# Optimization experiments

Measured on AMD Instinct MI355X. Metric: run time of the kernel, lower is better.

## Reference

```python
import jax, jax.numpy as jnp
import numpy as np

H = 4  # fixed number of heads in the layer


def setup_inputs() -> dict:
    key = jax.random.key(0)
    ks = jax.random.split(key, 6)
    B, S, D = 4, 2048, 512
    U = 2 * D  # per-head projection width (units = d_model * 2)
    x = jax.random.normal(ks[0], (B, S, D), dtype=jnp.float32)
    gamma = jnp.ones((D,), dtype=jnp.float32)
    beta = jnp.zeros((D,), dtype=jnp.float32)
    s = 0.02
    Wq = jax.random.normal(ks[1], (H, D, U), dtype=jnp.float32) * s
    Wk = jax.random.normal(ks[2], (H, D, U), dtype=jnp.float32) * s
    Wv = jax.random.normal(ks[3], (H, D, U), dtype=jnp.float32) * s
    Wout = jax.random.normal(ks[4], (H * U, D), dtype=jnp.float32) * s
    return {"x": x, "gamma": gamma, "beta": beta, "Wq": Wq, "Wk": Wk, "Wv": Wv, "Wout": Wout}


def _forward(x, gamma, beta, Wq, Wk, Wv, Wout):
    B, S, D = x.shape
    eps = 1e-6
    # LayerNormalization over last axis (Keras default, eps=1e-6)
    mu = jnp.mean(x, axis=-1, keepdims=True)
    var = jnp.mean(jnp.square(x - mu), axis=-1, keepdims=True)
    xn = (x - mu) * jax.lax.rsqrt(var + eps) * gamma + beta
    # Per-head Q/K/V projections, batched over head axis. Dropout is identity at inference.
    q = jnp.einsum('bsd,hdu->bhsu', xn, Wq)
    k = jnp.einsum('bsd,hdu->bhsu', xn, Wk)
    v = jnp.einsum('bsd,hdu->bhsu', xn, Wv)
    # Keras Attention(use_scale=False, causal=True): unscaled dot-product scores
    scores = jnp.einsum('bhsu,bhtu->bhst', q, k)  # [B,H,S,S]
    causal = jnp.tril(jnp.ones((S, S), dtype=bool))
    scores = jnp.where(causal, scores, jnp.finfo(scores.dtype).min)
    probs = jax.nn.softmax(scores, axis=-1)
    head = jnp.einsum('bhst,bhtu->bhsu', probs, v)  # [B,H,S,U]
    # concat heads in head order -> [B,S,H*U], then output Dense back to D
    HU = head.shape[1] * head.shape[3]
    cat = head.transpose(0, 2, 1, 3).reshape(B, S, HU)
    return cat @ Wout


def reference(x, gamma, beta, Wq, Wk, Wv, Wout):
    return _forward(x, gamma, beta, Wq, Wk, Wv, Wout)
```

## Files before the change

### kernel.cpp

```cpp
#include <hip/hip_runtime.h>

typedef _Float16 half8 __attribute__((ext_vector_type(8)));
typedef float floatx4 __attribute__((ext_vector_type(4)));

__device__ __forceinline__ void gl16(const _Float16* g, _Float16* l) {
    __builtin_amdgcn_global_load_lds((const __attribute__((address_space(1))) void*)g,
                                     (__attribute__((address_space(3))) void*)l, 16, 0, 0);
}

__device__ __forceinline__ half8 dsr16(const _Float16* p) {
    half8 r;
    const __attribute__((address_space(3))) _Float16* lp =
        (const __attribute__((address_space(3))) _Float16*)p;
    asm volatile("ds_read_b128 %0, %1" : "=v"(r) : "v"(lp));
    return r;
}

#define Scst 2048
#define Dcst 512
#define Ucst 1024
#define Hcst 4
#define SDo 1048576LL
#define UDo 524288LL
#define SUo 2097152LL
#define SSo 4194304LL
#define USo 2097152LL
#define SHUo 8388608LL

__global__ __launch_bounds__(64) void ln_k(const float* __restrict__ x,
                                           const float* __restrict__ gamma,
                                           const float* __restrict__ beta,
                                           _Float16* __restrict__ xn) {
    const int D = 512;
    long long base = (long long)blockIdx.x * D;
    int lane = threadIdx.x;
    floatx4 x0 = *(const floatx4*)(x + base + lane * 8);
    floatx4 x1 = *(const floatx4*)(x + base + lane * 8 + 4);
    float f[8];
#pragma unroll
    for (int i = 0; i < 4; i++) { f[i] = x0[i]; f[4 + i] = x1[i]; }
    float s = 0.f, ss = 0.f;
#pragma unroll
    for (int i = 0; i < 8; i++) { s += f[i]; ss += f[i] * f[i]; }
#pragma unroll
    for (int off = 32; off; off >>= 1) { s += __shfl_xor(s, off); ss += __shfl_xor(ss, off); }
    float mean = s * (1.f / 512.f);
    float var = ss * (1.f / 512.f) - mean * mean;
    float rstd = rsqrtf(var + 1e-6f);
    floatx4 g0 = *(const floatx4*)(gamma + lane * 8);
    floatx4 g1 = *(const floatx4*)(gamma + lane * 8 + 4);
    floatx4 b0 = *(const floatx4*)(beta + lane * 8);
    floatx4 b1 = *(const floatx4*)(beta + lane * 8 + 4);
    half8 o;
#pragma unroll
    for (int i = 0; i < 4; i++) {
        o[i]     = (_Float16)((f[i]     - mean) * rstd * g0[i] + b0[i]);
        o[4 + i] = (_Float16)((f[4 + i] - mean) * rstd * g1[i] + b1[i]);
    }
    *(half8*)(xn + base + lane * 8) = o;
}

__global__ __launch_bounds__(256) void tr_k(const float* __restrict__ in,
                                            _Float16* __restrict__ out, int R, int C) {
    __shared__ _Float16 tile[32][33];
    int tx = threadIdx.x, ty = threadIdx.y;
    long long zo = (long long)blockIdx.z * R * C;
    int r0 = blockIdx.y * 32, c0 = blockIdx.x * 32;
    for (int yy = ty; yy < 32; yy += 8)
        tile[yy][tx] = (_Float16)in[zo + (long long)(r0 + yy) * C + c0 + tx];
    __syncthreads();
    for (int yy = ty; yy < 32; yy += 8)
        out[zo + (long long)(c0 + yy) * R + r0 + tx] = tile[tx][yy];
}

#define BM 128
#define BN 128
#define BK 32
__global__ __launch_bounds__(256) void gemm_bt(
    const _Float16* __restrict__ A, const _Float16* __restrict__ Bt, void* __restrict__ Cv,
    int K, int ldc, int cflags, int mode) {
    int z = blockIdx.z;
    long long offA = 0, offB = 0, offC = 0;
    switch (mode) {
        case 1:
            offA = (long long)((z >> 2) & 1) * SDo;
            offB = (long long)(((z >> 3) * 4) + (z & 3)) * UDo;
            offC = (long long)(((z >> 3) * 8) + ((z & 3) * 2) + ((z >> 2) & 1)) * SUo;
            break;
        case 2:
            offA = (long long)z * SUo; offB = (long long)z * SUo; offC = (long long)z * SSo;
            break;
        case 3:
            offA = (long long)(z >> 1) * UDo; offB = (long long)(z & 1) * SDo;
            offC = (long long)z * USo;
            break;
        case 4:
            offA = (long long)z * SSo; offB = (long long)z * USo;
            offC = (long long)(z & 1) * SHUo + (long long)(z >> 1) * Ucst;
            break;
        case 6:
            offB = (long long)(z & 7) * UDo; offC = (long long)z * SUo;
            break;
        case 7:
            offA = (long long)(z & 3) * UDo; offC = (long long)z * USo;
            break;
        default: break;
    }
    const _Float16* Ab = A + offA;
    const _Float16* Bb = Bt + offB;

    int gx = gridDim.x, gy = gridDim.y;
    int nb = gx * gy;
    int lin = blockIdx.y * gx + blockIdx.x;
    int mIdx, nIdx;
    if (((nb & 7) == 0) && ((gx & 3) == 0)) {
        int chunk = nb >> 3;
        int vid = (lin >> 3) + chunk * (lin & 7);
        int panelH = gy * 4;
        int panel = vid / panelH;
        int rem = vid - panel * panelH;
        mIdx = rem >> 2;
        nIdx = (panel << 2) + (rem & 3);
    } else { mIdx = blockIdx.y; nIdx = blockIdx.x; }
    int m0 = mIdx * BM, n0 = nIdx * BN;

    if ((cflags & 4) && n0 > m0 + (BM - 1)) return;
    int kend = (cflags & 8) ? min(K, m0 + BM) : K;

    __shared__ _Float16 As[2][BM * BK];
    __shared__ _Float16 Bs[2][BN * BK];

    int t = threadIdx.x;
    int srow = t >> 2;
    int scol = (t & 3) * 8;
    int lane = t & 63, w = t >> 6;
    int wm = (w >> 1) * 64, wn = (w & 1) * 64;
    int lm = lane & 15, lk = (lane >> 4) * 8;

    floatx4 acc[4][4];
#pragma unroll
    for (int i = 0; i < 4; i++)
#pragma unroll
        for (int j = 0; j < 4; j++) acc[i][j] = floatx4{0.f, 0.f, 0.f, 0.f};

    const _Float16* ga0 = Ab + (long long)(m0 + srow) * K + scol;
    const _Float16* ga1 = Ab + (long long)(m0 + 64 + srow) * K + scol;
    const _Float16* gb0 = Bb + (long long)(n0 + srow) * K + scol;
    const _Float16* gb1 = Bb + (long long)(n0 + 64 + srow) * K + scol;

    int nIter = kend / BK;
    gl16(ga0, &As[0][t * 8]);
    gl16(ga1, &As[0][2048 + t * 8]);
    gl16(gb0, &Bs[0][t * 8]);
    gl16(gb1, &Bs[0][2048 + t * 8]);

    for (int it = 0; it < nIter; it++) {
        __syncthreads();
        int cur = it & 1;
        half8 af[4], bfr[4];
#pragma unroll
        for (int i = 0; i < 4; i++) af[i] = *(const half8*)&As[cur][(wm + i * 16 + lm) * BK + lk];
#pragma unroll
        for (int j = 0; j < 4; j++) bfr[j] = *(const half8*)&Bs[cur][(wn + j * 16 + lm) * BK + lk];
        if (it + 1 < nIter) {
            int nk = (it + 1) * BK;
            int nxt = cur ^ 1;
            gl16(ga0 + nk, &As[nxt][t * 8]);
            gl16(ga1 + nk, &As[nxt][2048 + t * 8]);
            gl16(gb0 + nk, &Bs[nxt][t * 8]);
            gl16(gb1 + nk, &Bs[nxt][2048 + t * 8]);
        }
#pragma unroll
        for (int i = 0; i < 4; i++)
#pragma unroll
            for (int j = 0; j < 4; j++)
                acc[i][j] = __builtin_amdgcn_mfma_f32_16x16x32_f16(af[i], bfr[j], acc[i][j], 0, 0, 0);
    }

    int cr = (lane >> 4) * 4;
    int cc = lm;
    bool outf32 = (cflags & 1) != 0;
#pragma unroll
    for (int i = 0; i < 4; i++) {
#pragma unroll
        for (int j = 0; j < 4; j++) {
            int rr = m0 + wm + i * 16 + cr;
            int nn = n0 + wn + j * 16 + cc;
#pragma unroll
            for (int r2 = 0; r2 < 4; r2++) {
                long long idx = (long long)(rr + r2) * ldc + nn + offC;
                float val = acc[i][j][r2];
                if (outf32) ((float*)Cv)[idx] = val;
                else ((_Float16*)Cv)[idx] = (_Float16)val;
            }
        }
    }
}

__global__ __launch_bounds__(512, 2) void gemm_bt256(
    const _Float16* __restrict__ A, const _Float16* __restrict__ Bt, void* __restrict__ Cv,
    int K, int ldc, int cflags, int mode) {
    int z = blockIdx.z;
    long long offA = 0, offB = 0, offC = 0;
    switch (mode) {
        case 1:
            offA = (long long)((z >> 2) & 1) * SDo;
            offB = (long long)(((z >> 3) * 4) + (z & 3)) * UDo;
            offC = (long long)(((z >> 3) * 8) + ((z & 3) * 2) + ((z >> 2) & 1)) * SUo;
            break;
        case 2:
            offA = (long long)z * SUo; offB = (long long)z * SUo; offC = (long long)z * SSo;
            break;
        case 3:
            offA = (long long)(z >> 1) * UDo; offB = (long long)(z & 1) * SDo;
            offC = (long long)z * USo;
            break;
        case 4:
            offA = (long long)z * SSo; offB = (long long)z * USo;
            offC = (long long)(z & 1) * SHUo + (long long)(z >> 1) * Ucst;
            break;
        default: break;
    }
    const _Float16* Ab = A + offA;
    const _Float16* Bb = Bt + offB;

    int gx = gridDim.x;
    int nwg = gx * gridDim.y;
    int lin = blockIdx.y * gx + blockIdx.x;
    int q8 = nwg >> 3, r8 = nwg & 7;
    int xcd = lin & 7, sub8 = lin >> 3;
    int wg = (xcd < r8 ? xcd * (q8 + 1) : r8 * (q8 + 1) + (xcd - r8) * q8) + sub8;
    int m0 = (wg / gx) * 256, n0 = (wg % gx) * 256;

    if ((cflags & 4) && n0 > m0 + 255) return;
    int kend = (cflags & 8) ? min(K, m0 + 256) : K;
    int NT = kend >> 6;

    __shared__ _Float16 As2[2][2][8192];
    __shared__ _Float16 Bs2[2][2][8192];

    int t = threadIdx.x;
    int lane = t & 63, w = t >> 6;
    int wm = (w >> 2) * 128, wn = (w & 3) * 64;
    int lm = lane & 15, ls = lane >> 4;
    int sw8 = ((ls ^ ((lm >> 1) & 3)) << 3);

    long long stoff = (long long)(t >> 2) * K + (((t & 3) ^ ((t >> 3) & 3)) << 3);
    const _Float16* gA = Ab + (long long)m0 * K + stoff;
    const _Float16* gB = Bb + (long long)n0 * K + stoff;
    long long rowK = 128LL * K;
    int ldd = t * 8;

    floatx4 acc[8][4];
#pragma unroll
    for (int i = 0; i < 8; i++)
#pragma unroll
        for (int j = 0; j < 4; j++) acc[i][j] = floatx4{0.f, 0.f, 0.f, 0.f};

#define STGA(v, ks) { const _Float16* s_ = gA + (((v) << 6) + ((ks) << 5)); \
        gl16(s_, &As2[(v) & 1][ks][ldd]); gl16(s_ + rowK, &As2[(v) & 1][ks][4096 + ldd]); }
#define STGB(v, ks) { const _Float16* s_ = gB + (((v) << 6) + ((ks) << 5)); \
        gl16(s_, &Bs2[(v) & 1][ks][ldd]); gl16(s_ + rowK, &Bs2[(v) & 1][ks][4096 + ldd]); }
#define RDA(mm, ks) dsr16(&As2[cur][ks][(wm + (mm) * 16 + lm) * 32 + sw8])
#define RDB(nn, ks) dsr16(&Bs2[cur][ks][(wn + (nn) * 16 + lm) * 32 + sw8])
#define MFMAH(m0_, m1_) \
    _Pragma("unroll") for (int mm = (m0_); mm < (m1_); mm++) \
    _Pragma("unroll") for (int nn = 0; nn < 4; nn++) \
        acc[mm][nn] = __builtin_amdgcn_mfma_f32_16x16x32_f16( \
            af[mm], bf[nn], acc[mm][nn], 0, 0, 0);

    STGA(0, 0) STGB(0, 0) STGA(0, 1) STGB(0, 1) STGA(1, 0) STGB(1, 0)
    asm volatile("s_waitcnt vmcnt(8)" ::: "memory");
    __builtin_amdgcn_s_barrier();

    for (int tt = 0; tt < NT; tt++) {
        int cur = tt & 1;
        half8 af[8], bf[4];
        bool more = (tt + 1 < NT);
        bf[0] = RDB(0, 0); bf[1] = RDB(1, 0); bf[2] = RDB(2, 0); bf[3] = RDB(3, 0);
        af[0] = RDA(0, 0); af[1] = RDA(1, 0); af[2] = RDA(2, 0); af[3] = RDA(3, 0);
        af[4] = RDA(4, 0); af[5] = RDA(5, 0); af[6] = RDA(6, 0); af[7] = RDA(7, 0);
        if (more) asm volatile("s_waitcnt vmcnt(4)" ::: "memory");
        else      asm volatile("s_waitcnt vmcnt(0)" ::: "memory");
        __builtin_amdgcn_s_barrier();
        asm volatile("s_waitcnt lgkmcnt(4)" ::: "memory");
        __builtin_amdgcn_sched_barrier(0);
        __builtin_amdgcn_s_setprio(1);
        MFMAH(0, 4)
        asm volatile("s_waitcnt lgkmcnt(0)" ::: "memory");
        __builtin_amdgcn_sched_barrier(0);
        MFMAH(4, 8)
        __builtin_amdgcn_s_setprio(0);
        if (more) { STGA(tt + 1, 1) STGB(tt + 1, 1) }
        bf[0] = RDB(0, 1); bf[1] = RDB(1, 1); bf[2] = RDB(2, 1); bf[3] = RDB(3, 1);
        af[0] = RDA(0, 1); af[1] = RDA(1, 1); af[2] = RDA(2, 1); af[3] = RDA(3, 1);
        af[4] = RDA(4, 1); af[5] = RDA(5, 1); af[6] = RDA(6, 1); af[7] = RDA(7, 1);
        if (more) asm volatile("s_waitcnt vmcnt(4)" ::: "memory");
        else      asm volatile("s_waitcnt vmcnt(0)" ::: "memory");
        __builtin_amdgcn_s_barrier();
        asm volatile("s_waitcnt lgkmcnt(4)" ::: "memory");
        __builtin_amdgcn_sched_barrier(0);
        __builtin_amdgcn_s_setprio(1);
        MFMAH(0, 4)
        asm volatile("s_waitcnt lgkmcnt(0)" ::: "memory");
        __builtin_amdgcn_sched_barrier(0);
        MFMAH(4, 8)
        __builtin_amdgcn_s_setprio(0);
        if (tt + 2 < NT) { STGA(tt + 2, 0) STGB(tt + 2, 0) }
    }

    int cr = ls * 4, cc = lm;
    bool outf32 = (cflags & 1) != 0;
#pragma unroll
    for (int i = 0; i < 8; i++) {
#pragma unroll
        for (int j = 0; j < 4; j++) {
            int rr = m0 + wm + i * 16 + cr;
            int nn = n0 + wn + j * 16 + cc;
#pragma unroll
            for (int r2 = 0; r2 < 4; r2++) {
                long long idx = (long long)(rr + r2) * ldc + nn + offC;
                float val = acc[i][j][r2];
                if (outf32) ((float*)Cv)[idx] = val;
                else ((_Float16*)Cv)[idx] = (_Float16)val;
            }
        }
    }
#undef STGA
#undef STGB
#undef RDA
#undef RDB
#undef MFMAH
}

__global__ __launch_bounds__(256) void softmax_h(_Float16* __restrict__ sc, int S) {
    int wid = threadIdx.x >> 6, lane = threadIdx.x & 63;
    int idx = blockIdx.x * 4 + wid;
    int r = idx & (S - 1);
    _Float16* srow = sc + (long long)idx * S;
    int nc = r >> 9;
    float v[32];
    float mx = -3.0e38f;
    for (int c = 0; c <= nc; c++) {
        half8 hv = *(half8*)(srow + lane * 8 + c * 512);
#pragma unroll
        for (int i = 0; i < 8; i++) {
            int n = lane * 8 + c * 512 + i;
            float s = (n <= r) ? (float)hv[i] : -3.0e38f;
            v[c * 8 + i] = s; mx = fmaxf(mx, s);
        }
    }
#pragma unroll
    for (int off = 32; off; off >>= 1) mx = fmaxf(mx, __shfl_xor(mx, off));
    float sum = 0.f;
    for (int c = 0; c <= nc; c++)
#pragma unroll
        for (int i = 0; i < 8; i++) {
            int n = lane * 8 + c * 512 + i;
            float e = (n <= r) ? __expf(v[c * 8 + i] - mx) : 0.f;
            v[c * 8 + i] = e; sum += e;
        }
#pragma unroll
    for (int off = 32; off; off >>= 1) sum += __shfl_xor(sum, off);
    float inv = 1.f / sum;
    for (int c = 0; c <= nc; c++) {
        half8 o;
#pragma unroll
        for (int i = 0; i < 8; i++) o[i] = (_Float16)(v[c * 8 + i] * inv);
        *(half8*)(srow + lane * 8 + c * 512) = o;
    }
}

extern "C" void kernel_launch(void* const* d_in, const int* in_sizes, int n_in,
                              void* d_out, int out_size, void* d_ws, size_t ws_size,
                              hipStream_t stream) {
    const int B = 4, S = 2048, D = 512, H = 4, U = 1024;
    const float* x     = (const float*)d_in[0];
    const float* gamma = (const float*)d_in[1];
    const float* beta  = (const float*)d_in[2];
    const float* Wq    = (const float*)d_in[3];
    const float* Wk    = (const float*)d_in[4];
    const float* Wv    = (const float*)d_in[5];
    const float* Wout  = (const float*)d_in[6];
    float* out = (float*)d_out;

    char* ws = (char*)d_ws;
    const size_t MiB = 1ull << 20;
    const long long SD = SDo, UD = UDo, SU = SUo, US = USo;

    _Float16* xn  = (_Float16*)(ws + 0);
    _Float16* WqT = (_Float16*)(ws + 8  * MiB);
    _Float16* WkT = (_Float16*)(ws + 12 * MiB);
    _Float16* WvT = (_Float16*)(ws + 16 * MiB);
    _Float16* WoT = (_Float16*)(ws + 20 * MiB);

    tr_k<<<dim3(U / 32, D / 32, H), dim3(32, 8), 0, stream>>>(Wq, WqT, D, U);
    tr_k<<<dim3(U / 32, D / 32, H), dim3(32, 8), 0, stream>>>(Wk, WkT, D, U);
    tr_k<<<dim3(U / 32, D / 32, H), dim3(32, 8), 0, stream>>>(Wv, WvT, D, U);
    tr_k<<<dim3(D / 32, (H * U) / 32, 1), dim3(32, 8), 0, stream>>>(Wout, WoT, H * U, D);
    ln_k<<<B * S, 64, 0, stream>>>(x, gamma, beta, xn);

    if (ws_size >= 168 * MiB) {
        _Float16* qk  = (_Float16*)(ws + 24 * MiB);
        _Float16* kk  = qk + 8 * SU;
        _Float16* sc  = (_Float16*)(ws + 88 * MiB);
        _Float16* vt  = qk;
        _Float16* cat = kk;

        for (int p = 0; p < 2; p++) {
            const _Float16* xnp = xn + (long long)p * 2 * SD;
            float* outp = out + (long long)p * 2 * SD;
            gemm_bt256<<<dim3(U / 256, S / 256, 16), 512, 0, stream>>>(xnp, WqT, qk, D, U, 0, 1);
            gemm_bt256<<<dim3(S / 256, S / 256, 8), 512, 0, stream>>>(qk, kk, sc, U, S, 4, 2);
            softmax_h<<<8 * S / 4, 256, 0, stream>>>(sc, S);
            gemm_bt256<<<dim3(S / 256, U / 256, 8), 512, 0, stream>>>(WvT, xnp, vt, D, S, 0, 3);
            gemm_bt256<<<dim3(U / 256, S / 256, 8), 512, 0, stream>>>(sc, vt, cat, S, H * U, 8, 4);
            gemm_bt<<<dim3(D / 128, 2 * S / 128, 1), 256, 0, stream>>>(cat, WoT, outp,
                H * U, D, 1, 0);
        }
    } else {
        _Float16* qb   = (_Float16*)(ws + 24 * MiB);
        _Float16* vTb  = (_Float16*)(ws + 56 * MiB);
        _Float16* catb = (_Float16*)(ws + 72 * MiB);
        _Float16* sc   = (_Float16*)(ws + 88 * MiB);

        for (int b = 0; b < B; b++) {
            const _Float16* xnb = xn + (long long)b * SD;
            gemm_bt<<<dim3(U / 128, S / 128, 2 * H), 256, 0, stream>>>(xnb, WqT, qb, D, U, 0, 6);
            gemm_bt<<<dim3(S / 128, U / 128, H), 256, 0, stream>>>(WvT, xnb, vTb, D, S, 0, 7);
            for (int h = 0; h < H; h++) {
                gemm_bt<<<dim3(S / 128, S / 128, 1), 256, 0, stream>>>(qb + (long long)h * SU,
                    qb + (long long)(H + h) * SU, sc, U, S, 4, 0);
                softmax_h<<<S / 4, 256, 0, stream>>>(sc, S);
                gemm_bt<<<dim3(U / 128, S / 128, 1), 256, 0, stream>>>(sc,
                    vTb + (long long)h * US, (void*)(catb + (long long)h * U), S, H * U, 8, 0);
            }
            gemm_bt<<<dim3(D / 128, S / 128, 1), 256, 0, stream>>>(catb, WoT,
                (void*)(out + (long long)b * SD), H * U, D, 1, 0);
        }
    }
}
```

Measured before the change: 696.5 us.

## Stage GEMM epilogue through LDS for coalesced fp16 stores and reorder prefetch

```diff
diff --git a/kernel.cpp b/kernel.cpp
--- a/kernel.cpp
+++ b/kernel.cpp
@@ -6,14 +6,6 @@
 __device__ __forceinline__ void gl16(const _Float16* g, _Float16* l) {
     __builtin_amdgcn_global_load_lds((const __attribute__((address_space(1))) void*)g,
                                      (__attribute__((address_space(3))) void*)l, 16, 0, 0);
-}
-
-__device__ __forceinline__ half8 dsr16(const _Float16* p) {
-    half8 r;
-    const __attribute__((address_space(3))) _Float16* lp =
-        (const __attribute__((address_space(3))) _Float16*)p;
-    asm volatile("ds_read_b128 %0, %1" : "=v"(r) : "v"(lp));
-    return r;
 }
 
 #define Scst 2048
@@ -236,8 +228,9 @@
     int kend = (cflags & 8) ? min(K, m0 + 256) : K;
     int NT = kend >> 6;
 
-    __shared__ _Float16 As2[2][2][8192];
-    __shared__ _Float16 Bs2[2][2][8192];
+    __shared__ _Float16 SH[65536];
+#define ASX(b, k, i) SH[((b) << 14) + ((k) << 13) + (i)]
+#define BSX(b, k, i) SH[32768 + ((b) << 14) + ((k) << 13) + (i)]
 
     int t = threadIdx.x;
     int lane = t & 63, w = t >> 6;
@@ -258,13 +251,13 @@
         for (int j = 0; j < 4; j++) acc[i][j] = floatx4{0.f, 0.f, 0.f, 0.f};
 
 #define STGA(v, ks) { const _Float16* s_ = gA + (((v) << 6) + ((ks) << 5)); \
-        gl16(s_, &As2[(v) & 1][ks][ldd]); gl16(s_ + rowK, &As2[(v) & 1][ks][4096 + ldd]); }
+        gl16(s_, &ASX((v) & 1, ks, ldd)); gl16(s_ + rowK, &ASX((v) & 1, ks, 4096 + ldd)); }
 #define STGB(v, ks) { const _Float16* s_ = gB + (((v) << 6) + ((ks) << 5)); \
-        gl16(s_, &Bs2[(v) & 1][ks][ldd]); gl16(s_ + rowK, &Bs2[(v) & 1][ks][4096 + ldd]); }
-#define RDA(mm, ks) dsr16(&As2[cur][ks][(wm + (mm) * 16 + lm) * 32 + sw8])
-#define RDB(nn, ks) dsr16(&Bs2[cur][ks][(wn + (nn) * 16 + lm) * 32 + sw8])
-#define MFMAH(m0_, m1_) \
-    _Pragma("unroll") for (int mm = (m0_); mm < (m1_); mm++) \
+        gl16(s_, &BSX((v) & 1, ks, ldd)); gl16(s_ + rowK, &BSX((v) & 1, ks, 4096 + ldd)); }
+#define RDA(mm, ks) (*(const half8*)&ASX(cur, ks, (wm + (mm) * 16 + lm) * 32 + sw8))
+#define RDB(nn, ks) (*(const half8*)&BSX(cur, ks, (wn + (nn) * 16 + lm) * 32 + sw8))
+#define MFMA32() \
+    _Pragma("unroll") for (int mm = 0; mm < 8; mm++) \
     _Pragma("unroll") for (int nn = 0; nn < 4; nn++) \
         acc[mm][nn] = __builtin_amdgcn_mfma_f32_16x16x32_f16( \
             af[mm], bf[nn], acc[mm][nn], 0, 0, 0);
@@ -275,62 +268,66 @@
 
     for (int tt = 0; tt < NT; tt++) {
         int cur = tt & 1;
-        half8 af[8], bf[4];
         bool more = (tt + 1 < NT);
-        bf[0] = RDB(0, 0); bf[1] = RDB(1, 0); bf[2] = RDB(2, 0); bf[3] = RDB(3, 0);
-        af[0] = RDA(0, 0); af[1] = RDA(1, 0); af[2] = RDA(2, 0); af[3] = RDA(3, 0);
-        af[4] = RDA(4, 0); af[5] = RDA(5, 0); af[6] = RDA(6, 0); af[7] = RDA(7, 0);
-        if (more) asm volatile("s_waitcnt vmcnt(4)" ::: "memory");
-        else      asm volatile("s_waitcnt vmcnt(0)" ::: "memory");
-        __builtin_amdgcn_s_barrier();
-        asm volatile("s_waitcnt lgkmcnt(4)" ::: "memory");
-        __builtin_amdgcn_sched_barrier(0);
-        __builtin_amdgcn_s_setprio(1);
-        MFMAH(0, 4)
-        asm volatile("s_waitcnt lgkmcnt(0)" ::: "memory");
-        __builtin_amdgcn_sched_barrier(0);
-        MFMAH(4, 8)
-        __builtin_amdgcn_s_setprio(0);
-        if (more) { STGA(tt + 1, 1) STGB(tt + 1, 1) }
-        bf[0] = RDB(0, 1); bf[1] = RDB(1, 1); bf[2] = RDB(2, 1); bf[3] = RDB(3, 1);
-        af[0] = RDA(0, 1); af[1] = RDA(1, 1); af[2] = RDA(2, 1); af[3] = RDA(3, 1);
-        af[4] = RDA(4, 1); af[5] = RDA(5, 1); af[6] = RDA(6, 1); af[7] = RDA(7, 1);
-        if (more) asm volatile("s_waitcnt vmcnt(4)" ::: "memory");
-        else      asm volatile("s_waitcnt vmcnt(0)" ::: "memory");
-        __builtin_amdgcn_s_barrier();
-        asm volatile("s_waitcnt lgkmcnt(4)" ::: "memory");
-        __builtin_amdgcn_sched_barrier(0);
-        __builtin_amdgcn_s_setprio(1);
-        MFMAH(0, 4)
-        asm volatile("s_waitcnt lgkmcnt(0)" ::: "memory");
-        __builtin_amdgcn_sched_barrier(0);
-        MFMAH(4, 8)
-        __builtin_amdgcn_s_setprio(0);
-        if (tt + 2 < NT) { STGA(tt + 2, 0) STGB(tt + 2, 0) }
-    }
-
-    int cr = ls * 4, cc = lm;
-    bool outf32 = (cflags & 1) != 0;
+        {
+            half8 af[8], bf[4];
+            bf[0] = RDB(0, 0); bf[1] = RDB(1, 0); bf[2] = RDB(2, 0); bf[3] = RDB(3, 0);
+            af[0] = RDA(0, 0); af[1] = RDA(1, 0); af[2] = RDA(2, 0); af[3] = RDA(3, 0);
+            af[4] = RDA(4, 0); af[5] = RDA(5, 0); af[6] = RDA(6, 0); af[7] = RDA(7, 0);
+            if (more) asm volatile("s_waitcnt vmcnt(4)" ::: "memory");
+            else      asm volatile("s_waitcnt vmcnt(0)" ::: "memory");
+            __builtin_amdgcn_s_barrier();
+            if (more) { STGA(tt + 1, 1) STGB(tt + 1, 1) }
+            __builtin_amdgcn_s_setprio(1);
+            MFMA32()
+            __builtin_amdgcn_s_setprio(0);
+        }
+        {
+            half8 af[8], bf[4];
+            bf[0] = RDB(0, 1); bf[1] = RDB(1, 1); bf[2] = RDB(2, 1); bf[3] = RDB(3, 1);
+            af[0] = RDA(0, 1); af[1] = RDA(1, 1); af[2] = RDA(2, 1); af[3] = RDA(3, 1);
+            af[4] = RDA(4, 1); af[5] = RDA(5, 1); af[6] = RDA(6, 1); af[7] = RDA(7, 1);
+            if (more) asm volatile("s_waitcnt vmcnt(4)" ::: "memory");
+            else      asm volatile("s_waitcnt vmcnt(0)" ::: "memory");
+            __builtin_amdgcn_s_barrier();
+            if (tt + 2 < NT) { STGA(tt + 2, 0) STGB(tt + 2, 0) }
+            __builtin_amdgcn_s_setprio(1);
+            MFMA32()
+            __builtin_amdgcn_s_setprio(0);
+        }
+    }
+
+    __builtin_amdgcn_s_barrier();
+    int cr = ls * 4;
 #pragma unroll
     for (int i = 0; i < 8; i++) {
 #pragma unroll
         for (int j = 0; j < 4; j++) {
-            int rr = m0 + wm + i * 16 + cr;
-            int nn = n0 + wn + j * 16 + cc;
 #pragma unroll
             for (int r2 = 0; r2 < 4; r2++) {
-                long long idx = (long long)(rr + r2) * ldc + nn + offC;
-                float val = acc[i][j][r2];
-                if (outf32) ((float*)Cv)[idx] = val;
-                else ((_Float16*)Cv)[idx] = (_Float16)val;
+                int row = wm + i * 16 + cr + r2;
+                int col = wn + j * 16 + lm;
+                SH[row * 256 + (col ^ ((row & 3) << 3))] = (_Float16)acc[i][j][r2];
             }
         }
+    }
+    __builtin_amdgcn_s_barrier();
+    _Float16* Ch = (_Float16*)Cv;
+    int cchunk = t & 31;
+    int rbase = t >> 5;
+#pragma unroll
+    for (int it = 0; it < 16; it++) {
+        int r = rbase + it * 16;
+        half8 v = *(const half8*)&SH[r * 256 + ((cchunk ^ (r & 3)) << 3)];
+        *(half8*)&Ch[(long long)(m0 + r) * ldc + n0 + (cchunk << 3) + offC] = v;
     }
 #undef STGA
 #undef STGB
 #undef RDA
 #undef RDB
-#undef MFMAH
+#undef MFMA32
+#undef ASX
+#undef BSX
 }
 
 __global__ __launch_bounds__(256) void softmax_h(_Float16* __restrict__ sc, int S) {
```

After: 681.4 us. 2.2% less time.
